# Optimization experiments

Measured on AMD Instinct MI355X. Metric: run time of the kernel, lower is better.

Reference implementation:

```python
import jax, jax.numpy as jnp
import numpy as np

B, T, C = 4, 2048, 768
N_HEADS = 16
HEAD_DIM = C // N_HEADS  # 48
ROPE_BASE = 10000.0


def setup_inputs() -> dict:
    key = jax.random.key(0)
    ks = jax.random.split(key, 6)
    s = 0.02
    return {
        "hidden_states": jax.random.normal(ks[0], (B, T, C), dtype=jnp.float32),
        "attention_mask": jnp.ones((B, T), dtype=jnp.float32),
        "Wq": jax.random.normal(ks[1], (C, C), dtype=jnp.float32) * s,
        "bq": jnp.zeros((C,), dtype=jnp.float32),
        "Wk": jax.random.normal(ks[2], (C, C), dtype=jnp.float32) * s,
        "bk": jnp.zeros((C,), dtype=jnp.float32),
        "Wv": jax.random.normal(ks[3], (C, C), dtype=jnp.float32) * s,
        "bv": jnp.zeros((C,), dtype=jnp.float32),
        "Wo": jax.random.normal(ks[4], (C, C), dtype=jnp.float32) * s,
        "bo": jnp.zeros((C,), dtype=jnp.float32),
    }


def _rotate_half(x):
    x1, x2 = jnp.split(x, 2, axis=-1)
    return jnp.concatenate([-x2, x1], axis=-1)


def reference(hidden_states, attention_mask, Wq, bq, Wk, bk, Wv, bv, Wo, bo):
    b, t, c = hidden_states.shape
    h, d = N_HEADS, c // N_HEADS

    def split_heads(x):  # [b,t,c] -> [b,h,t,d]
        return x.reshape(b, t, h, d).transpose(0, 2, 1, 3)

    q = split_heads(hidden_states @ Wq.T + bq)
    k = split_heads(hidden_states @ Wk.T + bk)
    v = split_heads(hidden_states @ Wv.T + bv)

    # rotary embedding: cos/sin [t, d]
    pos = jnp.arange(t, dtype=jnp.float32)
    inv_freq = 1.0 / (ROPE_BASE ** (jnp.arange(0, d, 2, dtype=jnp.float32) / d))
    freqs = pos[:, None] * inv_freq[None, :]          # [t, d/2]
    emb = jnp.concatenate([freqs, freqs], axis=-1)    # [t, d]
    cos, sin = jnp.cos(emb), jnp.sin(emb)
    q = q * cos + _rotate_half(q) * sin
    k = k * cos + _rotate_half(k) * sin

    scores = jnp.einsum('bhqd,bhkd->bhqk', q, k) / jnp.sqrt(jnp.asarray(d, q.dtype))
    # additive padding mask: (1 - mask) * -10000, broadcast [b,1,1,t]
    scores = scores + (1.0 - attention_mask)[:, None, None, :] * -10000.0
    # causal mask with -inf
    causal = jnp.tril(jnp.ones((t, t), dtype=bool))
    scores = jnp.where(causal[None, None], scores, -jnp.inf)

    probs = jax.nn.softmax(scores, axis=-1)
    ctx = jnp.einsum('bhqk,bhkd->bhqd', probs, v)
    ctx = ctx.transpose(0, 2, 1, 3).reshape(b, t, c)
    return ctx @ Wo.T + bo
```

## Files before the change

### kernel.cpp

```cpp
#include <hip/hip_runtime.h>
#include <hip/hip_bf16.h>
#include <math.h>

#define BB 4
#define TT 2048
#define CC 768
#define NHD 16
#define HD 48
#define NQT 32

typedef __hip_bfloat16 bf16;
typedef __attribute__((ext_vector_type(8))) short short8;
typedef __attribute__((ext_vector_type(4))) float floatx4;

__device__ __forceinline__ unsigned short f2bf(float x) {
    bf16 h = __float2bfloat16(x);
    return *(unsigned short*)&h;
}
__device__ __forceinline__ float bfu2f(unsigned short u) {
    return __uint_as_float(((unsigned)u) << 16);
}

__device__ __forceinline__ void gl_lds16(const void* g, void* s) {
    __builtin_amdgcn_global_load_lds((const __attribute__((address_space(1))) void*)g,
                                     (__attribute__((address_space(3))) void*)s, 16, 0, 0);
}

__device__ __forceinline__ unsigned int pk_bf2(float a, float b) {
    unsigned int ua = __float_as_uint(a) + 0x8000u;
    unsigned int ub = __float_as_uint(b) + 0x8000u;
    return __builtin_amdgcn_perm(ub, ua, 0x07060302);
}

__device__ __forceinline__ unsigned int cvtpk(float lo, float hi) {
    unsigned int r;
    asm("v_cvt_pk_bf16_f32 %0, %1, %2" : "=v"(r) : "v"(lo), "v"(hi));
    return r;
}

#define HOT_BARRIER() asm volatile("s_waitcnt lgkmcnt(0)\n\ts_barrier" ::: "memory")

__global__ __launch_bounds__(256) void cast_hs(const float* __restrict__ src,
                                               unsigned short* __restrict__ dst) {
    int i = (blockIdx.x * 256 + threadIdx.x) * 4;
    float4 v = *(const float4*)(src + i);
    ushort4 p;
    p.x = f2bf(v.x); p.y = f2bf(v.y); p.z = f2bf(v.z); p.w = f2bf(v.w);
    *(ushort4*)(dst + i) = p;
}

__global__ __launch_bounds__(256) void cast_w4(const float* __restrict__ s0, const float* __restrict__ s1,
                                               const float* __restrict__ s2, const float* __restrict__ s3,
                                               unsigned short* __restrict__ d0, unsigned short* __restrict__ d1,
                                               unsigned short* __restrict__ d2, unsigned short* __restrict__ d3) {
    const float* s; unsigned short* d;
    switch (blockIdx.y) {
        case 0: s = s0; d = d0; break;
        case 1: s = s1; d = d1; break;
        case 2: s = s2; d = d2; break;
        default: s = s3; d = d3; break;
    }
    int i = (blockIdx.x * 256 + threadIdx.x) * 4;
    float4 v = *(const float4*)(s + i);
    ushort4 p;
    p.x = f2bf(v.x); p.y = f2bf(v.y); p.z = f2bf(v.z); p.w = f2bf(v.w);
    *(ushort4*)(d + i) = p;
}

__global__ __launch_bounds__(256) void rope_table(float2* __restrict__ tab) {
    int idx = blockIdx.x * 256 + threadIdx.x;
    int t = idx / 24, p = idx % 24;
    float inv_freq = powf(10000.0f, -((float)(2 * p) / (float)HD));
    float ang = (float)t * inv_freq;
    float sn, cs;
    sincosf(ang, &sn, &cs);
    tab[idx] = make_float2(cs, sn);
}

template <int MODE>
__global__ __launch_bounds__(256) void gemm_mfma(const unsigned short* __restrict__ A,
                                                 const unsigned short* __restrict__ Bw,
                                                 const float* __restrict__ b0p,
                                                 const float* __restrict__ b1p,
                                                 const float* __restrict__ b2p,
                                                 void* __restrict__ out0,
                                                 void* __restrict__ out1,
                                                 void* __restrict__ out2) {
    __shared__ __align__(16) unsigned short As[128][64];
    __shared__ __align__(16) unsigned short Bs[128][64];
    const int tid = threadIdx.x;
    const int w = tid >> 6, lane = tid & 63;
    const int quad = lane >> 4, ln = lane & 15;
    const int wr = w >> 1, wc = w & 1;

    const int NXB = (MODE == 1) ? 18 : 6;
    const int bx = blockIdx.x;
    const int xcd = bx & 7, slot = bx >> 3;
    const int n0 = (slot % NXB) * 128;
    const int m0 = ((slot / NXB) * 8 + xcd) * 128;

    const int srow = lane >> 3;
    const int ssw = ((lane & 7) ^ srow) * 8;
    const unsigned short* agp[4];
    const unsigned short* bgp[4];
    void* asl[4];
    void* bsl[4];
#pragma unroll
    for (int i = 0; i < 4; ++i) {
        const int R = i * 32 + w * 8;
        agp[i] = A + (size_t)(m0 + R + srow) * CC + ssw;
        bgp[i] = Bw + (size_t)(n0 + R + srow) * CC + ssw;
        asl[i] = &As[R][0];
        bsl[i] = &Bs[R][0];
    }

    floatx4 acc[4][4];
#pragma unroll
    for (int mi = 0; mi < 4; ++mi)
#pragma unroll
        for (int ni = 0; ni < 4; ++ni) acc[mi][ni] = (floatx4){0.f, 0.f, 0.f, 0.f};

    const int ps0 = (quad ^ (ln & 7)) * 8;

    for (int k0 = 0; k0 < CC; k0 += 64) {
        __syncthreads();
#pragma unroll
        for (int i = 0; i < 4; ++i) {
            gl_lds16(agp[i] + k0, asl[i]);
            gl_lds16(bgp[i] + k0, bsl[i]);
        }
        __syncthreads();
#pragma unroll
        for (int kh = 0; kh < 2; ++kh) {
            const int ps = ps0 ^ (kh * 32);
            short8 af[4], bfr[4];
#pragma unroll
            for (int mi = 0; mi < 4; ++mi)
                af[mi] = *(const short8*)&As[wr * 64 + mi * 16 + ln][ps];
#pragma unroll
            for (int ni = 0; ni < 4; ++ni)
                bfr[ni] = *(const short8*)&Bs[wc * 64 + ni * 16 + ln][ps];
#pragma unroll
            for (int mi = 0; mi < 4; ++mi)
#pragma unroll
                for (int ni = 0; ni < 4; ++ni)
                    acc[mi][ni] = __builtin_amdgcn_mfma_f32_16x16x32_bf16(af[mi], bfr[ni], acc[mi][ni], 0, 0, 0);
        }
    }

    if (MODE == 0) {
        float* outf = (float*)out0;
        float bv[4];
#pragma unroll
        for (int ni = 0; ni < 4; ++ni) bv[ni] = b0p[n0 + wc * 64 + ni * 16 + ln];
#pragma unroll
        for (int mi = 0; mi < 4; ++mi)
#pragma unroll
            for (int r = 0; r < 4; ++r) {
                size_t row = m0 + wr * 64 + mi * 16 + quad * 4 + r;
#pragma unroll
                for (int ni = 0; ni < 4; ++ni)
                    outf[row * CC + n0 + wc * 64 + ni * 16 + ln] = acc[mi][ni][r] + bv[ni];
            }
    } else {
        const int seg = n0 / CC;
        const int nl0 = n0 - seg * CC;
        const float* bp = (seg == 0) ? b0p : (seg == 1) ? b1p : b2p;
        float bv[4];
#pragma unroll
        for (int ni = 0; ni < 4; ++ni) bv[ni] = bp[nl0 + wc * 64 + ni * 16 + ln];

        if (seg < 2) {
            unsigned short* outb = (unsigned short*)(seg == 0 ? out0 : out1);
#pragma unroll
            for (int mi = 0; mi < 4; ++mi)
#pragma unroll
                for (int r = 0; r < 4; ++r) {
                    size_t row = m0 + wr * 64 + mi * 16 + quad * 4 + r;
#pragma unroll
                    for (int ni = 0; ni < 4; ++ni)
                        outb[row * CC + nl0 + wc * 64 + ni * 16 + ln] = f2bf(acc[mi][ni][r] + bv[ni]);
                }
        } else {
            unsigned short* outb = (unsigned short*)out2;
            const int b = m0 >> 11;
#pragma unroll
            for (int ni = 0; ni < 4; ++ni) {
                int col = nl0 + wc * 64 + ni * 16 + ln;
                int h = col / HD, d = col % HD;
                size_t base = (size_t)((b * NHD + h) * HD + d) * TT;
#pragma unroll
                for (int mi = 0; mi < 4; ++mi) {
                    int t = (m0 & 2047) + wr * 64 + mi * 16 + quad * 4;
                    ushort4 pk;
                    pk.x = f2bf(acc[mi][ni][0] + bv[ni]);
                    pk.y = f2bf(acc[mi][ni][1] + bv[ni]);
                    pk.z = f2bf(acc[mi][ni][2] + bv[ni]);
                    pk.w = f2bf(acc[mi][ni][3] + bv[ni]);
                    *(ushort4*)(outb + base + t) = pk;
                }
            }
        }
    }
}

__global__ __launch_bounds__(256) void rope_bf(unsigned short* __restrict__ q,
                                               unsigned short* __restrict__ k,
                                               const float2* __restrict__ tab) {
    int idx = blockIdx.x * blockDim.x + threadIdx.x;
    const int HALF = HD / 2;
    int p8 = idx % 3;
    int rest = idx / 3;
    int h = rest % NHD;
    int n = rest / NHD;
    int t = n & (TT - 1);
    const float QSC = 0.14433756729740643f * 1.4426950408889634f;
    size_t base = (size_t)n * CC + h * HD + p8 * 8;
    const float2* tp = tab + t * HALF + p8 * 8;

    short8 q1 = *(const short8*)(q + base);
    short8 q2 = *(const short8*)(q + base + HALF);
    short8 k1 = *(const short8*)(k + base);
    short8 k2 = *(const short8*)(k + base + HALF);
    short8 r1, r2, s1, s2;
#pragma unroll
    for (int jj = 0; jj < 8; ++jj) {
        float2 cssn = tp[jj];
        float cs = cssn.x, sn = cssn.y;
        float a = bfu2f((unsigned short)q1[jj]), bb = bfu2f((unsigned short)q2[jj]);
        r1[jj] = (short)f2bf((a * cs - bb * sn) * QSC);
        r2[jj] = (short)f2bf((bb * cs + a * sn) * QSC);
        float c2 = bfu2f((unsigned short)k1[jj]), d2 = bfu2f((unsigned short)k2[jj]);
        s1[jj] = (short)f2bf(c2 * cs - d2 * sn);
        s2[jj] = (short)f2bf(d2 * cs + c2 * sn);
    }
    *(short8*)(q + base) = r1;
    *(short8*)(q + base + HALF) = r2;
    *(short8*)(k + base) = s1;
    *(short8*)(k + base + HALF) = s2;
}

__global__ __launch_bounds__(128, 2) void attn_kernel(const unsigned short* __restrict__ qb,
                                                      const unsigned short* __restrict__ kb,
                                                      const unsigned short* __restrict__ vt,
                                                      const float* __restrict__ amask,
                                                      unsigned short* __restrict__ ctx) {
    const int bx = blockIdx.x;
    const int xcd = bx & 7;
    const int s = bx >> 3;
    const int bh_l = s & 7;
    const int pairidx = s >> 3;
    const int j = (bh_l << 3) | xcd;
    const int b = j >> 4, h = j & 15;
    const int tid = threadIdx.x;
    const int w = tid >> 6, lane = tid & 63;
    const int g = lane >> 4, ln = lane & 15;
    const int sw = ln & 7;

    __shared__ __align__(16) unsigned short Ks[64][64];
    __shared__ __align__(16) unsigned short Vs[48][64];
    __shared__ __align__(16) unsigned short Pw[2][32][64];
    __shared__ __align__(16) float l_s[2][32];

    const short8 z8 = {0, 0, 0, 0, 0, 0, 0, 0};
    const short8 ones8 = {0x3F80, 0x3F80, 0x3F80, 0x3F80, 0x3F80, 0x3F80, 0x3F80, 0x3F80};

    {
        int rr = tid & 63, half = tid >> 6;
        *(short8*)&Ks[rr][((6 + half) ^ (rr & 7)) * 8] = z8;
    }

    const int u0 = tid, u1 = tid + 128, u2 = tid + 256;
    const int rK0 = u0 / 6, sK0 = u0 % 6;
    const int rK1 = u1 / 6, sK1 = u1 % 6;
    const int rK2 = u2 / 6, sK2 = u2 % 6;
    const int rV0 = u0 >> 3, sV0 = u0 & 7;
    const int rV1 = u1 >> 3, sV1 = u1 & 7;
    const int rV2 = u2 >> 3, sV2 = u2 & 7;
    unsigned short* dK0 = &Ks[rK0][(sK0 ^ (rK0 & 7)) * 8];
    unsigned short* dK1 = &Ks[rK1][(sK1 ^ (rK1 & 7)) * 8];
    unsigned short* dK2 = &Ks[rK2][(sK2 ^ (rK2 & 7)) * 8];
    unsigned short* dV0 = &Vs[rV0][(sV0 ^ (rV0 & 7)) * 8];
    unsigned short* dV1 = &Vs[rV1][(sV1 ^ (rV1 & 7)) * 8];
    unsigned short* dV2 = &Vs[rV2][(sV2 ^ (rV2 & 7)) * 8];
    const unsigned short* kbase0 = kb + (size_t)(b * TT + rK0) * CC + h * HD + sK0 * 8;
    const unsigned short* kbase1 = kb + (size_t)(b * TT + rK1) * CC + h * HD + sK1 * 8;
    const unsigned short* kbase2 = kb + (size_t)(b * TT + rK2) * CC + h * HD + sK2 * 8;
    const unsigned short* vbase0 = vt + ((size_t)((b * NHD + h) * HD) + rV0) * TT + sV0 * 8;
    const unsigned short* vbase1 = vt + ((size_t)((b * NHD + h) * HD) + rV1) * TT + sV1 * 8;
    const unsigned short* vbase2 = vt + ((size_t)((b * NHD + h) * HD) + rV2) * TT + sV2 * 8;
    const float* mbase = amask + b * TT + (tid & 63);
    const float MBS = -10000.0f * 1.4426950408889634f;
    const int mcol = (6 ^ (tid & 7)) * 8;
    const short8 vone = (ln == 0) ? ones8 : z8;
    const int rowA = w * 32 + ln;

    for (int rep = 0; rep < 2; ++rep) {
        const int qt = rep ? (NQT - 1 - pairidx) : pairidx;
        const int q0 = qt * 64;

        const unsigned short* qrA = qb + (size_t)(b * TT + q0 + w * 32 + ln) * CC + h * HD;
        const unsigned short* qrB = qrA + (size_t)16 * CC;
        short8 aq0a = *(const short8*)(qrA + g * 8);
        short8 aq0b = *(const short8*)(qrB + g * 8);
        short8 aq1a, aq1b;
        if (g < 2) {
            aq1a = *(const short8*)(qrA + 32 + g * 8);
            aq1b = *(const short8*)(qrB + 32 + g * 8);
        } else {
            aq1a = z8; aq1b = z8;
            if (g == 2) { aq1a[0] = (short)0x3F80; aq1b[0] = (short)0x3F80; }
        }

        const unsigned short* kp0 = kbase0;
        const unsigned short* kp1 = kbase1;
        const unsigned short* kp2 = kbase2;
        const unsigned short* vp0 = vbase0;
        const unsigned short* vp1 = vbase1;
        const unsigned short* vp2 = vbase2;
        const float* mp = mbase;

        short8 kr0 = *(const short8*)kp0;
        short8 kr1 = *(const short8*)kp1;
        short8 kr2 = *(const short8*)kp2;
        short8 vr0 = *(const short8*)vp0;
        short8 vr1 = *(const short8*)vp1;
        short8 vr2 = *(const short8*)vp2;
        float mr = (tid < 64) ? *mp : 1.0f;

        floatx4 oa0 = {0.f, 0.f, 0.f, 0.f}, oa1 = oa0, oa2 = oa0, oa3 = oa0;
        floatx4 ob0 = oa0, ob1 = oa0, ob2 = oa0, ob3 = oa0;

        for (int kt = 0; kt <= qt; ++kt) {
            HOT_BARRIER();
            *(short8*)dK0 = kr0; *(short8*)dK1 = kr1; *(short8*)dK2 = kr2;
            *(short8*)dV0 = vr0; *(short8*)dV1 = vr1; *(short8*)dV2 = vr2;
            if (tid < 64) Ks[tid][mcol] = f2bf((1.0f - mr) * MBS);
            HOT_BARRIER();

            if (kt < qt) {
                kp0 += (size_t)64 * CC; kr0 = *(const short8*)kp0;
                kp1 += (size_t)64 * CC; kr1 = *(const short8*)kp1;
                kp2 += (size_t)64 * CC; kr2 = *(const short8*)kp2;
                vp0 += 64; vr0 = *(const short8*)vp0;
                vp1 += 64; vr1 = *(const short8*)vp1;
                vp2 += 64; vr2 = *(const short8*)vp2;
                if (tid < 64) { mp += 64; mr = *mp; }
            }

            const bool masked = (kt == qt);

            floatx4 sa_[4], sb_[4];
#pragma unroll
            for (int c = 0; c < 4; ++c) {
                short8 kf0 = *(const short8*)&Ks[c * 16 + ln][(g ^ sw) * 8];
                short8 kf1 = *(const short8*)&Ks[c * 16 + ln][((4 + g) ^ sw) * 8];
                floatx4 z = {0.f, 0.f, 0.f, 0.f};
                floatx4 za = __builtin_amdgcn_mfma_f32_16x16x32_bf16(kf0, aq0a, z, 0, 0, 0);
                sa_[c] = __builtin_amdgcn_mfma_f32_16x16x32_bf16(kf1, aq1a, za, 0, 0, 0);
                floatx4 zb = __builtin_amdgcn_mfma_f32_16x16x32_bf16(kf0, aq0b, z, 0, 0, 0);
                sb_[c] = __builtin_amdgcn_mfma_f32_16x16x32_bf16(kf1, aq1b, zb, 0, 0, 0);
            }

#pragma unroll
            for (int c = 0; c < 4; ++c) {
                float pva[4], pvb[4];
#pragma unroll
                for (int r = 0; r < 4; ++r) {
                    pva[r] = __builtin_amdgcn_exp2f(sa_[c][r]);
                    pvb[r] = __builtin_amdgcn_exp2f(sb_[c][r]);
                }
                if (masked) {
#pragma unroll
                    for (int r = 0; r < 4; ++r) {
                        int kcol = c * 16 + g * 4 + r;
                        if (kcol > rowA) pva[r] = 0.f;
                        if (kcol > rowA + 16) pvb[r] = 0.f;
                    }
                }
                uint2 pka, pkb;
                pka.x = cvtpk(pva[0], pva[1]);
                pka.y = cvtpk(pva[2], pva[3]);
                pkb.x = cvtpk(pvb[0], pvb[1]);
                pkb.y = cvtpk(pvb[2], pvb[3]);
                *(uint2*)&Pw[w][ln][((2 * c + (g >> 1)) ^ sw) * 8 + (g & 1) * 4] = pka;
                *(uint2*)&Pw[w][16 + ln][((2 * c + (g >> 1)) ^ sw) * 8 + (g & 1) * 4] = pkb;
            }

            short8 pa0a = *(const short8*)&Pw[w][ln][(g ^ sw) * 8];
            short8 pa1a = *(const short8*)&Pw[w][ln][((4 + g) ^ sw) * 8];
            short8 pa0b = *(const short8*)&Pw[w][16 + ln][(g ^ sw) * 8];
            short8 pa1b = *(const short8*)&Pw[w][16 + ln][((4 + g) ^ sw) * 8];

#pragma unroll
            for (int n = 0; n < 3; ++n) {
                short8 vb0 = *(const short8*)&Vs[n * 16 + ln][(g ^ sw) * 8];
                short8 vb1 = *(const short8*)&Vs[n * 16 + ln][((4 + g) ^ sw) * 8];
                floatx4 acc = (n == 0) ? oa0 : (n == 1) ? oa1 : oa2;
                acc = __builtin_amdgcn_mfma_f32_16x16x32_bf16(pa0a, vb0, acc, 0, 0, 0);
                acc = __builtin_amdgcn_mfma_f32_16x16x32_bf16(pa1a, vb1, acc, 0, 0, 0);
                if (n == 0) oa0 = acc; else if (n == 1) oa1 = acc; else oa2 = acc;
                floatx4 accb = (n == 0) ? ob0 : (n == 1) ? ob1 : ob2;
                accb = __builtin_amdgcn_mfma_f32_16x16x32_bf16(pa0b, vb0, accb, 0, 0, 0);
                accb = __builtin_amdgcn_mfma_f32_16x16x32_bf16(pa1b, vb1, accb, 0, 0, 0);
                if (n == 0) ob0 = accb; else if (n == 1) ob1 = accb; else ob2 = accb;
            }
            oa3 = __builtin_amdgcn_mfma_f32_16x16x32_bf16(pa0a, vone, oa3, 0, 0, 0);
            oa3 = __builtin_amdgcn_mfma_f32_16x16x32_bf16(pa1a, vone, oa3, 0, 0, 0);
            ob3 = __builtin_amdgcn_mfma_f32_16x16x32_bf16(pa0b, vone, ob3, 0, 0, 0);
            ob3 = __builtin_amdgcn_mfma_f32_16x16x32_bf16(pa1b, vone, ob3, 0, 0, 0);
        }

        if (ln == 0) {
            *(floatx4*)&l_s[w][g * 4] = oa3;
            *(floatx4*)&l_s[w][16 + g * 4] = ob3;
        }
        floatx4 l4a = *(const floatx4*)&l_s[w][g * 4];
        floatx4 l4b = *(const floatx4*)&l_s[w][16 + g * 4];
#pragma unroll
        for (int r = 0; r < 4; ++r) {
            float invA = 1.0f / l4a[r];
            int t = q0 + w * 32 + g * 4 + r;
            unsigned short* dst = ctx + (size_t)(b * TT + t) * CC + h * HD;
            dst[ln] = f2bf(oa0[r] * invA);
            dst[16 + ln] = f2bf(oa1[r] * invA);
            dst[32 + ln] = f2bf(oa2[r] * invA);
            float invB = 1.0f / l4b[r];
            unsigned short* dstB = dst + (size_t)16 * CC;
            dstB[ln] = f2bf(ob0[r] * invB);
            dstB[16 + ln] = f2bf(ob1[r] * invB);
            dstB[32 + ln] = f2bf(ob2[r] * invB);
        }
    }
}

extern "C" void kernel_launch(void* const* d_in, const int* in_sizes, int n_in,
                              void* d_out, int out_size, void* d_ws, size_t ws_size,
                              hipStream_t stream) {
    const float* hs = (const float*)d_in[0];
    const float* amask = (const float*)d_in[1];
    const float* Wq = (const float*)d_in[2];
    const float* bq = (const float*)d_in[3];
    const float* Wk = (const float*)d_in[4];
    const float* bk = (const float*)d_in[5];
    const float* Wv = (const float*)d_in[6];
    const float* bv = (const float*)d_in[7];
    const float* Wo = (const float*)d_in[8];
    const float* bo = (const float*)d_in[9];

    const size_t NELEM = (size_t)BB * TT * CC;
    const size_t WELEM = (size_t)CC * CC;
    unsigned short* hb  = (unsigned short*)d_ws;
    unsigned short* qbuf = hb + NELEM;
    unsigned short* kbuf = qbuf + NELEM;
    unsigned short* vtb = kbuf + NELEM;
    unsigned short* ctxb = vtb + NELEM;
    unsigned short* wqb = ctxb + NELEM;
    unsigned short* wkb = wqb + WELEM;
    unsigned short* wvb = wkb + WELEM;
    unsigned short* wob = wvb + WELEM;
    float2* ropetab = (float2*)(wob + WELEM);

    cast_hs<<<NELEM / 1024, 256, 0, stream>>>(hs, hb);
    dim3 wgrid(WELEM / 1024, 4);
    cast_w4<<<wgrid, 256, 0, stream>>>(Wq, Wk, Wv, Wo, wqb, wkb, wvb, wob);
    rope_table<<<(TT * (HD / 2)) / 256, 256, 0, stream>>>(ropetab);

    gemm_mfma<1><<<18 * 64, 256, 0, stream>>>(hb, wqb, bq, bk, bv, qbuf, kbuf, vtb);

    int rope_total = BB * TT * NHD * 3;
    rope_bf<<<rope_total / 256, 256, 0, stream>>>(qbuf, kbuf, ropetab);

    attn_kernel<<<1024, 128, 0, stream>>>(qbuf, kbuf, vtb, amask, ctxb);

    gemm_mfma<0><<<6 * 64, 256, 0, stream>>>(ctxb, wob, bo, nullptr, nullptr,
                                             (float*)d_out, nullptr, nullptr);
}
```

Measured before the change: 226.3 us.

## Double-buffer K/V shared tiles in attention to halve barriers per tile

```diff
diff --git a/kernel.cpp b/kernel.cpp
--- a/kernel.cpp
+++ b/kernel.cpp
@@ -257,8 +257,8 @@
     const int g = lane >> 4, ln = lane & 15;
     const int sw = ln & 7;
 
-    __shared__ __align__(16) unsigned short Ks[64][64];
-    __shared__ __align__(16) unsigned short Vs[48][64];
+    __shared__ __align__(16) unsigned short Ks[2][64][64];
+    __shared__ __align__(16) unsigned short Vs[2][48][64];
     __shared__ __align__(16) unsigned short Pw[2][32][64];
     __shared__ __align__(16) float l_s[2][32];
 
@@ -267,7 +267,8 @@
 
     {
         int rr = tid & 63, half = tid >> 6;
-        *(short8*)&Ks[rr][((6 + half) ^ (rr & 7)) * 8] = z8;
+        *(short8*)&Ks[0][rr][((6 + half) ^ (rr & 7)) * 8] = z8;
+        *(short8*)&Ks[1][rr][((6 + half) ^ (rr & 7)) * 8] = z8;
     }
 
     const int u0 = tid, u1 = tid + 128, u2 = tid + 256;
@@ -277,12 +278,14 @@
     const int rV0 = u0 >> 3, sV0 = u0 & 7;
     const int rV1 = u1 >> 3, sV1 = u1 & 7;
     const int rV2 = u2 >> 3, sV2 = u2 & 7;
-    unsigned short* dK0 = &Ks[rK0][(sK0 ^ (rK0 & 7)) * 8];
-    unsigned short* dK1 = &Ks[rK1][(sK1 ^ (rK1 & 7)) * 8];
-    unsigned short* dK2 = &Ks[rK2][(sK2 ^ (rK2 & 7)) * 8];
-    unsigned short* dV0 = &Vs[rV0][(sV0 ^ (rV0 & 7)) * 8];
-    unsigned short* dV1 = &Vs[rV1][(sV1 ^ (rV1 & 7)) * 8];
-    unsigned short* dV2 = &Vs[rV2][(sV2 ^ (rV2 & 7)) * 8];
+    const int offK0 = rK0 * 64 + (sK0 ^ (rK0 & 7)) * 8;
+    const int offK1 = rK1 * 64 + (sK1 ^ (rK1 & 7)) * 8;
+    const int offK2 = rK2 * 64 + (sK2 ^ (rK2 & 7)) * 8;
+    const int offV0 = rV0 * 64 + (sV0 ^ (rV0 & 7)) * 8;
+    const int offV1 = rV1 * 64 + (sV1 ^ (rV1 & 7)) * 8;
+    const int offV2 = rV2 * 64 + (sV2 ^ (rV2 & 7)) * 8;
+    const int offM = (tid & 63) * 64 + (6 ^ (tid & 7)) * 8;
+
     const unsigned short* kbase0 = kb + (size_t)(b * TT + rK0) * CC + h * HD + sK0 * 8;
     const unsigned short* kbase1 = kb + (size_t)(b * TT + rK1) * CC + h * HD + sK1 * 8;
     const unsigned short* kbase2 = kb + (size_t)(b * TT + rK2) * CC + h * HD + sK2 * 8;
@@ -291,7 +294,6 @@
     const unsigned short* vbase2 = vt + ((size_t)((b * NHD + h) * HD) + rV2) * TT + sV2 * 8;
     const float* mbase = amask + b * TT + (tid & 63);
     const float MBS = -10000.0f * 1.4426950408889634f;
-    const int mcol = (6 ^ (tid & 7)) * 8;
     const short8 vone = (ln == 0) ? ones8 : z8;
     const int rowA = w * 32 + ln;
 
@@ -328,15 +330,25 @@
         short8 vr2 = *(const short8*)vp2;
         float mr = (tid < 64) ? *mp : 1.0f;
 
+        HOT_BARRIER();
+        {
+            unsigned short* kd = &Ks[0][0][0];
+            unsigned short* vd = &Vs[0][0][0];
+            *(short8*)(kd + offK0) = kr0;
+            *(short8*)(kd + offK1) = kr1;
+            *(short8*)(kd + offK2) = kr2;
+            *(short8*)(vd + offV0) = vr0;
+            *(short8*)(vd + offV1) = vr1;
+            *(short8*)(vd + offV2) = vr2;
+            if (tid < 64) kd[offM] = f2bf((1.0f - mr) * MBS);
+        }
+        HOT_BARRIER();
+
         floatx4 oa0 = {0.f, 0.f, 0.f, 0.f}, oa1 = oa0, oa2 = oa0, oa3 = oa0;
         floatx4 ob0 = oa0, ob1 = oa0, ob2 = oa0, ob3 = oa0;
 
         for (int kt = 0; kt <= qt; ++kt) {
-            HOT_BARRIER();
-            *(short8*)dK0 = kr0; *(short8*)dK1 = kr1; *(short8*)dK2 = kr2;
-            *(short8*)dV0 = vr0; *(short8*)dV1 = vr1; *(short8*)dV2 = vr2;
-            if (tid < 64) Ks[tid][mcol] = f2bf((1.0f - mr) * MBS);
-            HOT_BARRIER();
+            const int buf = kt & 1;
 
             if (kt < qt) {
                 kp0 += (size_t)64 * CC; kr0 = *(const short8*)kp0;
@@ -353,8 +365,8 @@
             floatx4 sa_[4], sb_[4];
 #pragma unroll
             for (int c = 0; c < 4; ++c) {
-                short8 kf0 = *(const short8*)&Ks[c * 16 + ln][(g ^ sw) * 8];
-                short8 kf1 = *(const short8*)&Ks[c * 16 + ln][((4 + g) ^ sw) * 8];
+                short8 kf0 = *(const short8*)&Ks[buf][c * 16 + ln][(g ^ sw) * 8];
+                short8 kf1 = *(const short8*)&Ks[buf][c * 16 + ln][((4 + g) ^ sw) * 8];
                 floatx4 z = {0.f, 0.f, 0.f, 0.f};
                 floatx4 za = __builtin_amdgcn_mfma_f32_16x16x32_bf16(kf0, aq0a, z, 0, 0, 0);
                 sa_[c] = __builtin_amdgcn_mfma_f32_16x16x32_bf16(kf1, aq1a, za, 0, 0, 0);
@@ -394,8 +406,8 @@
 
 #pragma unroll
             for (int n = 0; n < 3; ++n) {
-                short8 vb0 = *(const short8*)&Vs[n * 16 + ln][(g ^ sw) * 8];
-                short8 vb1 = *(const short8*)&Vs[n * 16 + ln][((4 + g) ^ sw) * 8];
+                short8 vb0 = *(const short8*)&Vs[buf][n * 16 + ln][(g ^ sw) * 8];
+                short8 vb1 = *(const short8*)&Vs[buf][n * 16 + ln][((4 + g) ^ sw) * 8];
                 floatx4 acc = (n == 0) ? oa0 : (n == 1) ? oa1 : oa2;
                 acc = __builtin_amdgcn_mfma_f32_16x16x32_bf16(pa0a, vb0, acc, 0, 0, 0);
                 acc = __builtin_amdgcn_mfma_f32_16x16x32_bf16(pa1a, vb1, acc, 0, 0, 0);
@@ -409,6 +421,19 @@
             oa3 = __builtin_amdgcn_mfma_f32_16x16x32_bf16(pa1a, vone, oa3, 0, 0, 0);
             ob3 = __builtin_amdgcn_mfma_f32_16x16x32_bf16(pa0b, vone, ob3, 0, 0, 0);
             ob3 = __builtin_amdgcn_mfma_f32_16x16x32_bf16(pa1b, vone, ob3, 0, 0, 0);
+
+            if (kt < qt) {
+                unsigned short* kd = &Ks[buf ^ 1][0][0];
+                unsigned short* vd = &Vs[buf ^ 1][0][0];
+                *(short8*)(kd + offK0) = kr0;
+                *(short8*)(kd + offK1) = kr1;
+                *(short8*)(kd + offK2) = kr2;
+                *(short8*)(vd + offV0) = vr0;
+                *(short8*)(vd + offV1) = vr1;
+                *(short8*)(vd + offV2) = vr2;
+                if (tid < 64) kd[offM] = f2bf((1.0f - mr) * MBS);
+            }
+            HOT_BARRIER();
         }
 
         if (ln == 0) {
```

Result: no change. 223.9 us (-1.1%).
